# Performance work log

Hardware: AMD Instinct MI355X
Metric: run time of the kernel (lower is better)

Reference implementation:

```python
import jax, jax.numpy as jnp
import numpy as np

B, N, L, D = 16, 8192, 512, 384  # batch, points, latents, model dim
FF = 4 * D  # feedforward inner dim (after GEGLU split)


def _ln(x, g, b, eps=1e-5):
    m = jnp.mean(x, axis=-1, keepdims=True)
    v = jnp.mean((x - m) ** 2, axis=-1, keepdims=True)
    return (x - m) * jax.lax.rsqrt(v + eps) * g + b


def setup_inputs() -> dict:
    key = jax.random.key(0)
    ks = jax.random.split(key, 16)
    s = 0.02
    def w(k, shape):
        return jax.random.normal(k, shape, jnp.float32) * s
    return {
        "x": jax.random.normal(ks[0], (B, N, 3), jnp.float32),
        # MLP: in(3)->D, D->D, D->D, D->D with ReLU between (eqx-style depth=3)
        "mlp_w0": w(ks[1], (3, D)), "mlp_b0": jnp.zeros((D,), jnp.float32),
        "mlp_w1": w(ks[2], (D, D)), "mlp_b1": jnp.zeros((D,), jnp.float32),
        "mlp_w2": w(ks[3], (D, D)), "mlp_b2": jnp.zeros((D,), jnp.float32),
        "mlp_w3": w(ks[4], (D, D)), "mlp_b3": jnp.zeros((D,), jnp.float32),
        "query": jax.random.normal(ks[5], (1, L, D), jnp.float32),
        "ln_q_g": jnp.ones((D,), jnp.float32), "ln_q_b": jnp.zeros((D,), jnp.float32),
        "ln_ctx_g": jnp.ones((D,), jnp.float32), "ln_ctx_b": jnp.zeros((D,), jnp.float32),
        "wq": w(ks[6], (D, D)),
        "wkv": w(ks[7], (D, 2 * D)),
        "wo": w(ks[8], (D, D)), "bo": jnp.zeros((D,), jnp.float32),
        "ln_ff_g": jnp.ones((D,), jnp.float32), "ln_ff_b": jnp.zeros((D,), jnp.float32),
        "ff_w1": w(ks[9], (D, 2 * FF)), "ff_b1": jnp.zeros((2 * FF,), jnp.float32),
        "ff_w2": w(ks[10], (FF, D)), "ff_b2": jnp.zeros((D,), jnp.float32),
    }


def reference(x, mlp_w0, mlp_b0, mlp_w1, mlp_b1, mlp_w2, mlp_b2, mlp_w3, mlp_b3,
              query, ln_q_g, ln_q_b, ln_ctx_g, ln_ctx_b, wq, wkv, wo, bo,
              ln_ff_g, ln_ff_b, ff_w1, ff_b1, ff_w2, ff_b2):
    # point MLP: 3 -> D
    h = jax.nn.relu(x @ mlp_w0 + mlp_b0)
    h = jax.nn.relu(h @ mlp_w1 + mlp_b1)
    h = jax.nn.relu(h @ mlp_w2 + mlp_b2)
    ctx = h @ mlp_w3 + mlp_b3                      # [B, N, D]

    lq = jnp.broadcast_to(query, (x.shape[0], L, D))  # learnable latents

    # PreNorm cross-attention (heads=1, dim_head=D)
    qn = _ln(lq, ln_q_g, ln_q_b)
    cn = _ln(ctx, ln_ctx_g, ln_ctx_b)
    q = qn @ wq                                    # [B, L, D]
    kv = cn @ wkv
    k, v = jnp.split(kv, 2, axis=-1)               # [B, N, D] each
    scale = D ** -0.5
    sim = jnp.einsum('bid,bjd->bij', q, k) * scale # [B, L, N]
    attn = jax.nn.softmax(sim, axis=-1)
    out = jnp.einsum('bij,bjd->bid', attn, v)      # [B, L, D]
    x1 = (out @ wo + bo) + lq                      # residual

    # PreNorm GEGLU feedforward
    f = _ln(x1, ln_ff_g, ln_ff_b)
    f = f @ ff_w1 + ff_b1                          # [B, L, 2*FF]
    a, g = jnp.split(f, 2, axis=-1)
    f = a * jax.nn.gelu(g, approximate=False)      # GEGLU (exact gelu, torch default)
    return (f @ ff_w2 + ff_b2) + x1                # [B, L, D]
```

## Files before the change

### kernel.cpp

```cpp
#include <hip/hip_runtime.h>
#include <math.h>


typedef unsigned short u16;
typedef unsigned int   u32;
typedef __bf16 bf16_t;
typedef bf16_t bf16x8 __attribute__((ext_vector_type(8)));
typedef float  floatx4 __attribute__((ext_vector_type(4)));

__device__ __forceinline__ float b2f(u16 v) {
    return __uint_as_float(((u32)v) << 16);
}
__device__ __forceinline__ u16 f2b(float f) {
    bf16_t h = (bf16_t)f;
    return __builtin_bit_cast(u16, h);
}
__device__ __forceinline__ void stb4(u16* p, float4 f) {
    uint2 v;
    v.x = (u32)f2b(f.x) | ((u32)f2b(f.y) << 16);
    v.y = (u32)f2b(f.z) | ((u32)f2b(f.w) << 16);
    *(uint2*)p = v;
}

__device__ __forceinline__ void gl2lds16(u16* lds, const u16* g) {
    __builtin_amdgcn_global_load_lds(
        (const __attribute__((address_space(1))) void*)g,
        (__attribute__((address_space(3))) void*)lds, 16, 0, 0);
}

__device__ __forceinline__ void xcd_remap(int& bx, int& by, int& bz) {
    int gx = gridDim.x, gy = gridDim.y, gz = gridDim.z;
    int nb = gx * gy * gz;
    int p = bx + gx * (by + gy * bz);
    if ((nb & 7) == 0) {
        int chunk = nb >> 3;
        p = (p & 7) * chunk + (p >> 3);
    }
    bx = p % gx;
    int t = p / gx;
    by = t % gy;
    bz = t / gy;
}

__device__ __forceinline__ void xcd_remap_yf(int& bx, int& by, int& bz) {
    int gx = gridDim.x, gy = gridDim.y, gz = gridDim.z;
    int nb = gx * gy * gz;
    int p = by + gy * (bx + gx * bz);
    if ((nb & 7) == 0) {
        int chunk = nb >> 3;
        p = (p & 7) * chunk + (p >> 3);
    }
    by = p % gy;
    int t = p / gy;
    bx = t % gx;
    bz = t / gx;
}

__global__ __launch_bounds__(256) void wconv_all(
    const float* __restrict__ w1, const float* __restrict__ w2,
    const float* __restrict__ w3, const float* __restrict__ wq,
    const float* __restrict__ wkv, const float* __restrict__ wo,
    const float* __restrict__ ffw1, const float* __restrict__ ffw2,
    u16* __restrict__ d1, u16* __restrict__ d2, u16* __restrict__ d3,
    u16* __restrict__ dq, u16* __restrict__ dkv, u16* __restrict__ dо,
    u16* __restrict__ dffw1, u16* __restrict__ dffw2,
    u16* __restrict__ dwkd)
{
    int idx = blockIdx.x * 256 + threadIdx.x;
    if (idx >= 2949120) return;
    if (idx >= 2801664) {
        int local = idx - 2801664;
        int e = local / 384, d = local - e * 384;
        dwkd[local] = f2b(wkv[(long long)e * 768 + d]);
        return;
    }
    const float* W; u16* WT; int Kd, Nd, local;
    if      (idx <  147456) { W=w1;   WT=d1;    Kd=384;  Nd=384;  local=idx; }
    else if (idx <  294912) { W=w2;   WT=d2;    Kd=384;  Nd=384;  local=idx-147456; }
    else if (idx <  442368) { W=w3;   WT=d3;    Kd=384;  Nd=384;  local=idx-294912; }
    else if (idx <  589824) { W=wq;   WT=dq;    Kd=384;  Nd=384;  local=idx-442368; }
    else if (idx <  884736) { W=wkv;  WT=dkv;   Kd=384;  Nd=768;  local=idx-589824; }
    else if (idx < 1032192) { W=wo;   WT=dо;    Kd=384;  Nd=384;  local=idx-884736; }
    else if (idx < 2211840) { W=ffw1; WT=dffw1; Kd=384;  Nd=3072; local=idx-1032192; }
    else                    { W=ffw2; WT=dffw2; Kd=1536; Nd=384;  local=idx-2211840; }
    int n = local / Kd, k = local - n * Kd;
    WT[local] = f2b(W[(long long)k * Nd + n]);
}

__global__ __launch_bounds__(256) void layer0_kernel(
    const float* __restrict__ X, const float* __restrict__ W0,
    const float* __restrict__ B0, u16* __restrict__ H, int total4)
{
    int idx = blockIdx.x * 256 + threadIdx.x;
    if (idx >= total4) return;
    int e = idx * 4;
    int m = e / 384;
    int j = e - m * 384;
    float x0 = X[m * 3 + 0], x1 = X[m * 3 + 1], x2 = X[m * 3 + 2];
    float4 w0 = *(const float4*)(W0 + j);
    float4 w1 = *(const float4*)(W0 + 384 + j);
    float4 w2 = *(const float4*)(W0 + 768 + j);
    float4 bb = *(const float4*)(B0 + j);
    float4 v;
    v.x = fmaxf(bb.x + x0 * w0.x + x1 * w1.x + x2 * w2.x, 0.f);
    v.y = fmaxf(bb.y + x0 * w0.y + x1 * w1.y + x2 * w2.y, 0.f);
    v.z = fmaxf(bb.z + x0 * w0.z + x1 * w1.z + x2 * w2.z, 0.f);
    v.w = fmaxf(bb.w + x0 * w0.w + x1 * w1.w + x2 * w2.w, 0.f);
    stb4(H + e, v);
}

template<int IN_F32>
__global__ __launch_bounds__(256) void ln_kernel(
    const void* __restrict__ Xv, const float* __restrict__ g,
    const float* __restrict__ b, u16* __restrict__ Y, int rows)
{
    int w = threadIdx.x >> 6, lane = threadIdx.x & 63;
    int row = blockIdx.x * 4 + w;
    if (row >= rows) return;
    float v[6];
    float s = 0.f, ss = 0.f;
#pragma unroll
    for (int i = 0; i < 6; ++i) {
        int c = i * 64 + lane;
        v[i] = IN_F32 ? ((const float*)Xv)[(long long)row * 384 + c]
                      : b2f(((const u16*)Xv)[(long long)row * 384 + c]);
        s += v[i]; ss += v[i] * v[i];
    }
#pragma unroll
    for (int m = 32; m; m >>= 1) {
        s  += __shfl_xor(s, m, 64);
        ss += __shfl_xor(ss, m, 64);
    }
    float mean = s * (1.0f / 384.0f);
    float var  = ss * (1.0f / 384.0f) - mean * mean;
    float rs = rsqrtf(fmaxf(var, 0.f) + 1e-5f);
    u16* yr = Y + (long long)row * 384;
#pragma unroll
    for (int i = 0; i < 6; ++i) {
        int c = i * 64 + lane;
        yr[c] = f2b((v[i] - mean) * rs * g[c] + b[c]);
    }
}

#define STAGE_AB3(bufi, kk)                                                    \
    { u16* asd_ = shmem + (bufi) * 4096;                                       \
      u16* bsd_ = shmem + 12288 + (bufi) * 4096;                               \
      gl2lds16(asd_ + (wv * 32) * 32,                                          \
          aptr_ + (long long)(m0 + wv * 32 + rlo_) * lda_ + (kk) + c8_);       \
      gl2lds16(asd_ + (wv * 32 + 16) * 32,                                     \
          aptr_ + (long long)(m0 + wv * 32 + 16 + rlo_) * lda_ + (kk) + c8_);  \
      gl2lds16(bsd_ + (wv * 32) * 32,                                          \
          bptr_ + (long long)(n0 + wv * 32 + rlo_) * ldb_ + (kk) + c8_);       \
      gl2lds16(bsd_ + (wv * 32 + 16) * 32,                                     \
          bptr_ + (long long)(n0 + wv * 32 + 16 + rlo_) * ldb_ + (kk) + c8_); }

#define MFMA_TILE_PIPE(Aptr, Bptr, LDA, LDB, K0, K1)                           \
    {                                                                          \
        const u16* aptr_ = (Aptr); const u16* bptr_ = (Bptr);                  \
        const long long lda_ = (LDA), ldb_ = (LDB);                            \
        const int rlo_ = lane >> 2, c8_ = (lane & 3) * 8;                      \
        const int T_ = ((K1) - (K0)) >> 5;                                     \
        STAGE_AB3(0, (K0))                                                     \
        STAGE_AB3(1, (K0) + 32)                                                \
        int cur = 0;                                                           \
        for (int t = 0; t < T_; ++t) {                                         \
            if (t + 1 < T_) { asm volatile("s_waitcnt vmcnt(4)" ::: "memory"); } \
            else            { asm volatile("s_waitcnt vmcnt(0)" ::: "memory"); } \
            __builtin_amdgcn_s_barrier();                                      \
            if (t + 2 < T_) {                                                  \
                int stg = (cur == 0) ? 2 : cur - 1;                            \
                STAGE_AB3(stg, (K0) + (t + 2) * 32)                            \
            }                                                                  \
            const u16* As_ = shmem + cur * 4096;                               \
            const u16* Bs_ = shmem + 12288 + cur * 4096;                       \
            bf16x8 a0 = *(const bf16x8*)&As_[(wv * 32 + lr) * 32 + lq * 8];    \
            bf16x8 a1 = *(const bf16x8*)&As_[(wv * 32 + 16 + lr) * 32 + lq * 8]; \
            _Pragma("unroll")                                                  \
            for (int ns = 0; ns < 8; ++ns) {                                   \
                bf16x8 b = *(const bf16x8*)&Bs_[(ns * 16 + lr) * 32 + lq * 8]; \
                acc[0][ns] = __builtin_amdgcn_mfma_f32_16x16x32_bf16(a0, b, acc[0][ns], 0, 0, 0); \
                acc[1][ns] = __builtin_amdgcn_mfma_f32_16x16x32_bf16(a1, b, acc[1][ns], 0, 0, 0); \
            }                                                                  \
            cur = (cur == 2) ? 0 : cur + 1;                                    \
        }                                                                      \
    }

#define STAGE_AB2(bufi, kk)                                                    \
    { u16* asd_ = shmem + (bufi) * 4096;                                       \
      u16* bsd_ = shmem + 8192 + (bufi) * 4096;                                \
      gl2lds16(asd_ + (wv * 32) * 32,                                          \
          aptr_ + (long long)(m0 + wv * 32 + rlo_) * lda_ + (kk) + c8_);       \
      gl2lds16(asd_ + (wv * 32 + 16) * 32,                                     \
          aptr_ + (long long)(m0 + wv * 32 + 16 + rlo_) * lda_ + (kk) + c8_);  \
      gl2lds16(bsd_ + (wv * 32) * 32,                                          \
          bptr_ + (long long)(n0 + wv * 32 + rlo_) * ldb_ + (kk) + c8_);       \
      gl2lds16(bsd_ + (wv * 32 + 16) * 32,                                     \
          bptr_ + (long long)(n0 + wv * 32 + 16 + rlo_) * ldb_ + (kk) + c8_); }

#define MFMA_TILE_DBUF(Aptr, Bptr, LDA, LDB, K0, K1)                           \
    {                                                                          \
        const u16* aptr_ = (Aptr); const u16* bptr_ = (Bptr);                  \
        const long long lda_ = (LDA), ldb_ = (LDB);                            \
        const int rlo_ = lane >> 2, c8_ = (lane & 3) * 8;                      \
        int cur = 0;                                                           \
        STAGE_AB2(0, (K0))                                                     \
        for (int k0 = (K0); k0 < (K1); k0 += 32) {                             \
            __syncthreads();                                                   \
            if (k0 + 32 < (K1)) STAGE_AB2(cur ^ 1, k0 + 32)                    \
            const u16* As_ = shmem + cur * 4096;                               \
            const u16* Bs_ = shmem + 8192 + cur * 4096;                        \
            bf16x8 a0 = *(const bf16x8*)&As_[(wv * 32 + lr) * 32 + lq * 8];    \
            bf16x8 a1 = *(const bf16x8*)&As_[(wv * 32 + 16 + lr) * 32 + lq * 8]; \
            _Pragma("unroll")                                                  \
            for (int ns = 0; ns < 8; ++ns) {                                   \
                bf16x8 b = *(const bf16x8*)&Bs_[(ns * 16 + lr) * 32 + lq * 8]; \
                acc[0][ns] = __builtin_amdgcn_mfma_f32_16x16x32_bf16(a0, b, acc[0][ns], 0, 0, 0); \
                acc[1][ns] = __builtin_amdgcn_mfma_f32_16x16x32_bf16(a1, b, acc[1][ns], 0, 0, 0); \
            }                                                                  \
            cur ^= 1;                                                          \
        }                                                                      \
    }

template<int RES_F32, int OUT_F32>
__global__ __launch_bounds__(256) void gemm_mfma(
    const u16* __restrict__ A, const u16* __restrict__ WT,
    const float* __restrict__ bias, const void* __restrict__ res,
    void* __restrict__ C,
    int M, int N, int K, int lda, int ldb, int ldc, int ldres,
    float scale, int relu, int resmask,
    long long zsA, long long zsB, long long zsC)
{
    __shared__ u16 shmem[24576];
    const int tid = threadIdx.x;
    const int wv = tid >> 6, lane = tid & 63;
    const int lr = lane & 15, lq = lane >> 4;
    int bx = blockIdx.x, by = blockIdx.y, bz = blockIdx.z;
    xcd_remap_yf(bx, by, bz);
    const int m0 = bx * 128;
    const int n0 = by * 128;
    const u16* Az = A + bz * zsA;
    const u16* Bz = WT + bz * zsB;
    const long long czoff = bz * zsC;

    floatx4 acc[2][8];
#pragma unroll
    for (int i = 0; i < 2; ++i)
#pragma unroll
        for (int j = 0; j < 8; ++j)
            acc[i][j] = (floatx4){0.f, 0.f, 0.f, 0.f};

    MFMA_TILE_PIPE(Az, Bz, lda, ldb, 0, K)

    float bi[8];
#pragma unroll
    for (int ns = 0; ns < 8; ++ns)
        bi[ns] = bias ? bias[n0 + ns * 16 + lr] : 0.f;

#pragma unroll
    for (int ms = 0; ms < 2; ++ms) {
#pragma unroll
        for (int r = 0; r < 4; ++r) {
            int m = m0 + wv * 32 + ms * 16 + lq * 4 + r;
#pragma unroll
            for (int ns = 0; ns < 8; ++ns) {
                int col = n0 + ns * 16 + lr;
                float v = acc[ms][ns][r] * scale + bi[ns];
                if (relu) v = fmaxf(v, 0.f);
                if (res) {
                    long long ro = (long long)(m & resmask) * ldres + col;
                    v += RES_F32 ? ((const float*)res)[ro]
                                 : b2f(((const u16*)res)[ro]);
                }
                long long co = czoff + (long long)m * ldc + col;
                if (OUT_F32) ((float*)C)[co] = v;
                else         ((u16*)C)[co] = f2b(v);
            }
        }
    }
}

__global__ __launch_bounds__(256) void gemm_exp(
    const u16* __restrict__ A, const u16* __restrict__ WT,
    u16* __restrict__ P, float* __restrict__ den,
    int K, int lda, int ldb, int ldc,
    long long zsB, long long zsP)
{
    __shared__ u16 shmem[16384];
    const int tid = threadIdx.x;
    const int wv = tid >> 6, lane = tid & 63;
    const int lr = lane & 15, lq = lane >> 4;
    int bx = blockIdx.x, by = blockIdx.y, bz = blockIdx.z;
    xcd_remap(bx, by, bz);
    const int m0 = bx * 128;
    const int n0 = by * 128;
    const u16* Bz = WT + bz * zsB;
    u16* Pz = P + bz * zsP;
    float* dz = den + bz * 512;

    floatx4 acc[2][8];
#pragma unroll
    for (int i = 0; i < 2; ++i)
#pragma unroll
        for (int j = 0; j < 8; ++j)
            acc[i][j] = (floatx4){0.f, 0.f, 0.f, 0.f};

    MFMA_TILE_DBUF(A, Bz, lda, ldb, 0, K)

    u16* sh = shmem;
    float srow[2][4] = {};
#pragma unroll
    for (int ms = 0; ms < 2; ++ms) {
        __syncthreads();
#pragma unroll
        for (int ns = 0; ns < 8; ++ns)
#pragma unroll
            for (int r = 0; r < 4; ++r) {
                float l = acc[ms][ns][r];
                l = fminf(fmaxf(l, -60.f), 60.f);
                float p = __expf(l);
                srow[ms][r] += p;
                int row = wv * 16 + lq * 4 + r;
                int col = (ns * 16 + lr) ^ (((row >> 3) & 1) << 3);
                sh[row * 136 + col] = f2b(p);
            }
        __syncthreads();
#pragma unroll
        for (int j = 0; j < 4; ++j) {
            int idx = j * 256 + tid;
            int rl = idx >> 4, ch = idx & 15;
            int m = m0 + ((rl >> 4) << 5) + ms * 16 + (rl & 15);
            int src = rl * 136 + ((ch * 8) ^ ((((rl >> 3) & 1)) << 3));
            *(uint4*)&Pz[(long long)m * ldc + n0 + ch * 8] =
                *(const uint4*)&sh[src];
        }
    }
#pragma unroll
    for (int ms = 0; ms < 2; ++ms)
#pragma unroll
        for (int r = 0; r < 4; ++r) {
            float s = srow[ms][r];
            s += __shfl_xor(s, 1, 64);
            s += __shfl_xor(s, 2, 64);
            s += __shfl_xor(s, 4, 64);
            s += __shfl_xor(s, 8, 64);
            if (lr == 0)
                atomicAdd(&dz[m0 + wv * 32 + ms * 16 + lq * 4 + r], s);
        }
}

__global__ __launch_bounds__(256) void gemm_pv(
    const u16* __restrict__ P, const u16* __restrict__ VT,
    const float* __restrict__ den, u16* __restrict__ part, int SPLIT)
{
    __shared__ u16 shmem[24576];
    const int tid = threadIdx.x;
    const int wv = tid >> 6, lane = tid & 63;
    const int lr = lane & 15, lq = lane >> 4;
    int bx = blockIdx.x, by = blockIdx.y, bz = blockIdx.z;
    xcd_remap(bx, by, bz);
    const int m0 = bx * 128;
    const int n0 = by * 128;
    const int g = bz / SPLIT, sp = bz - g * SPLIT;
    const int chunk = 8192 / SPLIT;
    const u16* Az = P + (long long)g * 512 * 8192;
    const u16* Bz = VT + (long long)g * 384 * 8192;
    const float* dg = den + g * 512;

    floatx4 acc[2][8];
#pragma unroll
    for (int i = 0; i < 2; ++i)
#pragma unroll
        for (int j = 0; j < 8; ++j)
            acc[i][j] = (floatx4){0.f, 0.f, 0.f, 0.f};

    MFMA_TILE_PIPE(Az, Bz, 8192, 8192, sp * chunk, sp * chunk + chunk)

    u16* pz = part + (long long)bz * 512 * 384;
#pragma unroll
    for (int ms = 0; ms < 2; ++ms)
#pragma unroll
        for (int r = 0; r < 4; ++r) {
            int m = m0 + wv * 32 + ms * 16 + lq * 4 + r;
            float inv = 1.0f / dg[m];
#pragma unroll
            for (int ns = 0; ns < 8; ++ns) {
                int col = n0 + ns * 16 + lr;
                pz[(long long)m * 384 + col] = f2b(acc[ms][ns][r] * inv);
            }
        }
}

__global__ __launch_bounds__(256) void pv_reduce_kernel(
    const u16* __restrict__ part, u16* __restrict__ AO, int SPLIT)
{
    int idx = blockIdx.x * 256 + threadIdx.x;
    int q = idx / 96, j = (idx - q * 96) * 4;
    int g = q >> 9, ql = q & 511;
    const u16* base = part + ((long long)g * SPLIT * 512 + ql) * 384 + j;
    float4 s = make_float4(0.f, 0.f, 0.f, 0.f);
    for (int sp = 0; sp < SPLIT; ++sp) {
        uint2 v = *(const uint2*)(base + (long long)sp * 512 * 384);
        s.x += b2f((u16)(v.x & 0xffff));
        s.y += b2f((u16)(v.x >> 16));
        s.z += b2f((u16)(v.y & 0xffff));
        s.w += b2f((u16)(v.y >> 16));
    }
    stb4(AO + (long long)q * 384 + j, s);
}

__global__ __launch_bounds__(256) void gemm_ff1_geglu(
    const u16* __restrict__ A, const u16* __restrict__ WT,
    const float* __restrict__ bias, u16* __restrict__ C,
    int K, int lda, int ldb, int ldc)
{
    __shared__ u16 shmem[24576];
    const int tid = threadIdx.x;
    const int wv = tid >> 6, lane = tid & 63;
    const int lr = lane & 15, lq = lane >> 4;
    int bx = blockIdx.x, by = blockIdx.y, bz = blockIdx.z;
    xcd_remap_yf(bx, by, bz);
    const int m0 = bx * 128;
    const int n0 = by * 64;
    const int rlo = lane >> 2, c8 = (lane & 3) * 8;

    floatx4 accA[2][4], accG[2][4];
#pragma unroll
    for (int i = 0; i < 2; ++i)
#pragma unroll
        for (int j = 0; j < 4; ++j) {
            accA[i][j] = (floatx4){0.f, 0.f, 0.f, 0.f};
            accG[i][j] = (floatx4){0.f, 0.f, 0.f, 0.f};
        }

#define STAGE_FF(bufi, kk)                                                     \
    { u16* asd = shmem + (bufi) * 4096;                                        \
      u16* bsd = shmem + 12288 + (bufi) * 4096;                                \
      gl2lds16(asd + (wv * 32) * 32,                                           \
          A + (long long)(m0 + wv * 32 + rlo) * lda + (kk) + c8);              \
      gl2lds16(asd + (wv * 32 + 16) * 32,                                      \
          A + (long long)(m0 + wv * 32 + 16 + rlo) * lda + (kk) + c8);         \
      int r0 = wv * 32 + rlo, r1 = r0 + 16;                                    \
      int wrow0 = (r0 < 64) ? (n0 + r0) : (1536 + n0 + r0 - 64);               \
      int wrow1 = (r1 < 64) ? (n0 + r1) : (1536 + n0 + r1 - 64);               \
      gl2lds16(bsd + (wv * 32) * 32, WT + (long long)wrow0 * ldb + (kk) + c8); \
      gl2lds16(bsd + (wv * 32 + 16) * 32, WT + (long long)wrow1 * ldb + (kk) + c8); }

    const int T = K >> 5;
    STAGE_FF(0, 0)
    STAGE_FF(1, 32)
    int cur = 0;
    for (int t = 0; t < T; ++t) {
        if (t + 1 < T) { asm volatile("s_waitcnt vmcnt(4)" ::: "memory"); }
        else           { asm volatile("s_waitcnt vmcnt(0)" ::: "memory"); }
        __builtin_amdgcn_s_barrier();
        if (t + 2 < T) {
            int stg = (cur == 0) ? 2 : cur - 1;
            STAGE_FF(stg, (t + 2) * 32)
        }
        const u16* As_ = shmem + cur * 4096;
        const u16* Bs_ = shmem + 12288 + cur * 4096;
        bf16x8 a0 = *(const bf16x8*)&As_[(wv * 32 + lr) * 32 + lq * 8];
        bf16x8 a1 = *(const bf16x8*)&As_[(wv * 32 + 16 + lr) * 32 + lq * 8];
#pragma unroll
        for (int ns = 0; ns < 4; ++ns) {
            bf16x8 bA = *(const bf16x8*)&Bs_[(ns * 16 + lr) * 32 + lq * 8];
            bf16x8 bG = *(const bf16x8*)&Bs_[((64 + ns * 16) + lr) * 32 + lq * 8];
            accA[0][ns] = __builtin_amdgcn_mfma_f32_16x16x32_bf16(a0, bA, accA[0][ns], 0, 0, 0);
            accA[1][ns] = __builtin_amdgcn_mfma_f32_16x16x32_bf16(a1, bA, accA[1][ns], 0, 0, 0);
            accG[0][ns] = __builtin_amdgcn_mfma_f32_16x16x32_bf16(a0, bG, accG[0][ns], 0, 0, 0);
            accG[1][ns] = __builtin_amdgcn_mfma_f32_16x16x32_bf16(a1, bG, accG[1][ns], 0, 0, 0);
        }
        cur = (cur == 2) ? 0 : cur + 1;
    }
#undef STAGE_FF

    float ba[4], bg[4];
#pragma unroll
    for (int ns = 0; ns < 4; ++ns) {
        ba[ns] = bias[n0 + ns * 16 + lr];
        bg[ns] = bias[1536 + n0 + ns * 16 + lr];
    }
#pragma unroll
    for (int ms = 0; ms < 2; ++ms)
#pragma unroll
        for (int r = 0; r < 4; ++r) {
            int m = m0 + wv * 32 + ms * 16 + lq * 4 + r;
#pragma unroll
            for (int ns = 0; ns < 4; ++ns) {
                int col = n0 + ns * 16 + lr;
                float a = accA[ms][ns][r] + ba[ns];
                float g = accG[ms][ns][r] + bg[ns];
                float v = a * 0.5f * g * (1.0f + erff(g * 0.70710678118654752f));
                C[(long long)m * ldc + col] = f2b(v);
            }
        }
}

extern "C" void kernel_launch(void* const* d_in, const int* in_sizes, int n_in,
                              void* d_out, int out_size, void* d_ws, size_t ws_size,
                              hipStream_t stream) {
    const float* x     = (const float*)d_in[0];
    const float* w0    = (const float*)d_in[1];
    const float* b0    = (const float*)d_in[2];
    const float* w1    = (const float*)d_in[3];
    const float* b1    = (const float*)d_in[4];
    const float* w2    = (const float*)d_in[5];
    const float* b2    = (const float*)d_in[6];
    const float* w3    = (const float*)d_in[7];
    const float* b3    = (const float*)d_in[8];
    const float* query = (const float*)d_in[9];
    const float* lnqg  = (const float*)d_in[10];
    const float* lnqb  = (const float*)d_in[11];
    const float* lncg  = (const float*)d_in[12];
    const float* lncb  = (const float*)d_in[13];
    const float* wq    = (const float*)d_in[14];
    const float* wkv   = (const float*)d_in[15];
    const float* wo    = (const float*)d_in[16];
    const float* bo    = (const float*)d_in[17];
    const float* lnfg  = (const float*)d_in[18];
    const float* lnfb  = (const float*)d_in[19];
    const float* ffw1  = (const float*)d_in[20];
    const float* ffb1  = (const float*)d_in[21];
    const float* ffw2  = (const float*)d_in[22];
    const float* ffb2  = (const float*)d_in[23];
    float* out = (float*)d_out;
    char* wsb = (char*)d_ws;

    auto need = [](int G) -> size_t {
        return (size_t)G * (3LL * 6291456 + 8388608)
             + 25165824
             + 6291456
             + 3 * 393216 + 32768
             + 5898240;
    };
    int G = 2;
    if      (ws_size >= need(16)) G = 16;
    else if (ws_size >= need(8))  G = 8;
    else if (ws_size >= need(4))  G = 4;
    const int SPLIT = 64 / G;

    long long off = 0;
    u16*   bufA   = (u16*)(wsb + off); off += (long long)G * 6291456;
    u16*   bufB   = (u16*)(wsb + off); off += (long long)G * 6291456;
    u16*   VTb    = (u16*)(wsb + off); off += (long long)G * 6291456;
    u16*   Pb     = (u16*)(wsb + off); off += (long long)G * 8388608;
    u16*   part   = (u16*)(wsb + off); off += 25165824;
    u16*   ao_all = (u16*)(wsb + off); off += 6291456;
    u16*   qn     = (u16*)(wsb + off); off += 393216;
    u16*   qb     = (u16*)(wsb + off); off += 393216;
    u16*   q2     = (u16*)(wsb + off); off += 393216;
    float* den    = (float*)(wsb + off); off += 32768;
    u16*   w1T    = (u16*)(wsb + off); off += 294912;
    u16*   w2T    = (u16*)(wsb + off); off += 294912;
    u16*   w3T    = (u16*)(wsb + off); off += 294912;
    u16*   wqT    = (u16*)(wsb + off); off += 294912;
    u16*   wkvT   = (u16*)(wsb + off); off += 589824;
    u16*   woT    = (u16*)(wsb + off); off += 294912;
    u16*   ffw1T  = (u16*)(wsb + off); off += 2359296;
    u16*   ffw2T  = (u16*)(wsb + off); off += 1179648;
    u16*   wkdir  = (u16*)(wsb + off); off += 294912;
    u16*   x1_all = (u16*)(wsb + 0);
    u16*   f0_all = (u16*)(wsb + 6291456);
    u16*   gl_all = (u16*)(wsb + 12582912);

    const int FULLMASK = 0x3FFFFFFF;

    wconv_all<<<11520, 256, 0, stream>>>(w1, w2, w3, wq, wkv, wo, ffw1, ffw2,
        w1T, w2T, w3T, wqT, wkvT, woT, ffw1T, ffw2T, wkdir);
    hipMemsetAsync(den, 0, 16 * 512 * sizeof(float), stream);
    ln_kernel<1><<<128, 256, 0, stream>>>(query, lnqg, lnqb, qn, 512);
    gemm_mfma<0, 0><<<dim3(4, 3), 256, 0, stream>>>(qn, wqT, nullptr, nullptr, qb,
        512, 384, 384, 384, 384, 384, 0, 1.f, 0, FULLMASK, 0, 0, 0);
    gemm_mfma<0, 0><<<dim3(4, 3), 256, 0, stream>>>(qb, wkdir, nullptr, nullptr, q2,
        512, 384, 384, 384, 384, 384, 0, 0.05103103630798288f, 0, FULLMASK, 0, 0, 0);

    const int MG = G * 8192;
    for (int base = 0; base < 16; base += G) {
        const float* xg = x + (long long)base * 24576;

        layer0_kernel<<<G * 3072, 256, 0, stream>>>(xg, w0, b0, bufA, G * 786432);
        gemm_mfma<0, 0><<<dim3(MG / 128, 3), 256, 0, stream>>>(bufA, w1T, b1, nullptr, bufB,
            MG, 384, 384, 384, 384, 384, 0, 1.f, 1, FULLMASK, 0, 0, 0);
        gemm_mfma<0, 0><<<dim3(MG / 128, 3), 256, 0, stream>>>(bufB, w2T, b2, nullptr, bufA,
            MG, 384, 384, 384, 384, 384, 0, 1.f, 1, FULLMASK, 0, 0, 0);
        gemm_mfma<0, 0><<<dim3(MG / 128, 3), 256, 0, stream>>>(bufA, w3T, b3, nullptr, bufB,
            MG, 384, 384, 384, 384, 384, 0, 1.f, 0, FULLMASK, 0, 0, 0);
        ln_kernel<0><<<MG / 4, 256, 0, stream>>>(bufB, lncg, lncb, bufA, MG);
        gemm_mfma<0, 0><<<dim3(3, 64, G), 256, 0, stream>>>(wkvT + 147456, bufA,
            nullptr, nullptr, VTb, 384, 8192, 384, 384, 384, 8192, 0, 1.f, 0, FULLMASK,
            0, 8192LL * 384, 384LL * 8192);
        gemm_exp<<<dim3(4, 64, G), 256, 0, stream>>>(q2, bufA, Pb, den + base * 512,
            384, 384, 384, 8192, 8192LL * 384, 512LL * 8192);
        gemm_pv<<<dim3(4, 3, G * SPLIT), 256, 0, stream>>>(Pb, VTb, den + base * 512,
            part, SPLIT);
        pv_reduce_kernel<<<G * 192, 256, 0, stream>>>(part,
            ao_all + (long long)base * 196608, SPLIT);
    }

    gemm_mfma<1, 0><<<dim3(64, 3), 256, 0, stream>>>(ao_all, woT, bo, query, x1_all,
        8192, 384, 384, 384, 384, 384, 384, 1.f, 0, 511, 0, 0, 0);
    ln_kernel<0><<<2048, 256, 0, stream>>>(x1_all, lnfg, lnfb, f0_all, 8192);
    gemm_ff1_geglu<<<dim3(64, 24), 256, 0, stream>>>(f0_all, ffw1T, ffb1, gl_all,
        384, 384, 384, 1536);
    gemm_mfma<0, 1><<<dim3(64, 3), 256, 0, stream>>>(gl_all, ffw2T, ffb2, x1_all, out,
        8192, 384, 1536, 1536, 1536, 384, 384, 1.f, 0, FULLMASK, 0, 0, 0);
}
```

Measured before the change: 786.6 us.

## Fold value projection into output projection and fuse LN with transpose

Applies associativity: attention output times Wv times Wo is computed as attention output times a precomputed (Wv·Wo) matrix, so the per-batch V projection GEMM over all 8192 points is removed. The PV GEMM now consumes the transposed normalized context directly, and a new layernorm kernel writes both the normalized rows and their transpose through shared memory. This adds one small 384x384 weight GEMM and a strided transposed store, and changes bf16 rounding order slightly.

```diff
diff --git a/kernel.cpp b/kernel.cpp
--- a/kernel.cpp
+++ b/kernel.cpp
@@ -62,14 +62,20 @@
     const float* __restrict__ wkv, const float* __restrict__ wo,
     const float* __restrict__ ffw1, const float* __restrict__ ffw2,
     u16* __restrict__ d1, u16* __restrict__ d2, u16* __restrict__ d3,
-    u16* __restrict__ dq, u16* __restrict__ dkv, u16* __restrict__ dо,
+    u16* __restrict__ dq, u16* __restrict__ dо,
     u16* __restrict__ dffw1, u16* __restrict__ dffw2,
-    u16* __restrict__ dwkd)
+    u16* __restrict__ dwkd, u16* __restrict__ dwvd)
 {
     int idx = blockIdx.x * 256 + threadIdx.x;
-    if (idx >= 2949120) return;
-    if (idx >= 2801664) {
-        int local = idx - 2801664;
+    if (idx >= 2801664) return;
+    if (idx >= 2654208) {
+        int local = idx - 2654208;
+        int dd = local / 384, c = local - dd * 384;
+        dwvd[local] = f2b(wkv[(long long)dd * 768 + 384 + c]);
+        return;
+    }
+    if (idx >= 2506752) {
+        int local = idx - 2506752;
         int e = local / 384, d = local - e * 384;
         dwkd[local] = f2b(wkv[(long long)e * 768 + d]);
         return;
@@ -79,10 +85,9 @@
     else if (idx <  294912) { W=w2;   WT=d2;    Kd=384;  Nd=384;  local=idx-147456; }
     else if (idx <  442368) { W=w3;   WT=d3;    Kd=384;  Nd=384;  local=idx-294912; }
     else if (idx <  589824) { W=wq;   WT=dq;    Kd=384;  Nd=384;  local=idx-442368; }
-    else if (idx <  884736) { W=wkv;  WT=dkv;   Kd=384;  Nd=768;  local=idx-589824; }
-    else if (idx < 1032192) { W=wo;   WT=dо;    Kd=384;  Nd=384;  local=idx-884736; }
-    else if (idx < 2211840) { W=ffw1; WT=dffw1; Kd=384;  Nd=3072; local=idx-1032192; }
-    else                    { W=ffw2; WT=dffw2; Kd=1536; Nd=384;  local=idx-2211840; }
+    else if (idx <  737280) { W=wo;   WT=dо;    Kd=384;  Nd=384;  local=idx-589824; }
+    else if (idx < 1916928) { W=ffw1; WT=dffw1; Kd=384;  Nd=3072; local=idx-737280; }
+    else                    { W=ffw2; WT=dffw2; Kd=1536; Nd=384;  local=idx-1916928; }
     int n = local / Kd, k = local - n * Kd;
     WT[local] = f2b(W[(long long)k * Nd + n]);
 }
@@ -139,6 +144,54 @@
     for (int i = 0; i < 6; ++i) {
         int c = i * 64 + lane;
         yr[c] = f2b((v[i] - mean) * rs * g[c] + b[c]);
+    }
+}
+
+__global__ __launch_bounds__(256) void ln_tr_kernel(
+    const u16* __restrict__ Xv, const float* __restrict__ g,
+    const float* __restrict__ b, u16* __restrict__ Y, u16* __restrict__ YT)
+{
+    __shared__ u16 tr[384 * 72];
+    int w = threadIdx.x >> 6, lane = threadIdx.x & 63;
+    int row0 = blockIdx.x * 64;
+    for (int rr = 0; rr < 16; ++rr) {
+        int jl = w * 16 + rr;
+        long long row = row0 + jl;
+        float v[6];
+        float s = 0.f, ss = 0.f;
+#pragma unroll
+        for (int i = 0; i < 6; ++i) {
+            int c = i * 64 + lane;
+            v[i] = b2f(Xv[row * 384 + c]);
+            s += v[i]; ss += v[i] * v[i];
+        }
+#pragma unroll
+        for (int m = 32; m; m >>= 1) {
+            s  += __shfl_xor(s, m, 64);
+            ss += __shfl_xor(ss, m, 64);
+        }
+        float mean = s * (1.0f / 384.0f);
+        float var  = ss * (1.0f / 384.0f) - mean * mean;
+        float rs = rsqrtf(fmaxf(var, 0.f) + 1e-5f);
+        u16* yr = Y + row * 384;
+#pragma unroll
+        for (int i = 0; i < 6; ++i) {
+            int c = i * 64 + lane;
+            u16 val = f2b((v[i] - mean) * rs * g[c] + b[c]);
+            yr[c] = val;
+            tr[c * 72 + jl] = val;
+        }
+    }
+    __syncthreads();
+    int gb = row0 >> 13;
+    int jloc = row0 & 8191;
+    u16* yt = YT + (long long)gb * 384 * 8192 + jloc;
+    for (int e = threadIdx.x; e < 384; e += 256) {
+        const u16* src = &tr[e * 72];
+        u16* dst = yt + (long long)e * 8192;
+#pragma unroll
+        for (int q = 0; q < 8; ++q)
+            *(uint4*)(dst + q * 8) = *(const uint4*)(src + q * 8);
     }
 }
 
@@ -349,7 +402,7 @@
 }
 
 __global__ __launch_bounds__(256) void gemm_pv(
-    const u16* __restrict__ P, const u16* __restrict__ VT,
+    const u16* __restrict__ P, const u16* __restrict__ KT,
     const float* __restrict__ den, u16* __restrict__ part, int SPLIT)
 {
     __shared__ u16 shmem[24576];
@@ -363,7 +416,7 @@
     const int g = bz / SPLIT, sp = bz - g * SPLIT;
     const int chunk = 8192 / SPLIT;
     const u16* Az = P + (long long)g * 512 * 8192;
-    const u16* Bz = VT + (long long)g * 384 * 8192;
+    const u16* Bz = KT + (long long)g * 384 * 8192;
     const float* dg = den + g * 512;
 
     floatx4 acc[2][8];
@@ -542,7 +595,7 @@
     long long off = 0;
     u16*   bufA   = (u16*)(wsb + off); off += (long long)G * 6291456;
     u16*   bufB   = (u16*)(wsb + off); off += (long long)G * 6291456;
-    u16*   VTb    = (u16*)(wsb + off); off += (long long)G * 6291456;
+    u16*   knT    = (u16*)(wsb + off); off += (long long)G * 6291456;
     u16*   Pb     = (u16*)(wsb + off); off += (long long)G * 8388608;
     u16*   part   = (u16*)(wsb + off); off += 25165824;
     u16*   ao_all = (u16*)(wsb + off); off += 6291456;
@@ -554,25 +607,28 @@
     u16*   w2T    = (u16*)(wsb + off); off += 294912;
     u16*   w3T    = (u16*)(wsb + off); off += 294912;
     u16*   wqT    = (u16*)(wsb + off); off += 294912;
-    u16*   wkvT   = (u16*)(wsb + off); off += 589824;
     u16*   woT    = (u16*)(wsb + off); off += 294912;
     u16*   ffw1T  = (u16*)(wsb + off); off += 2359296;
     u16*   ffw2T  = (u16*)(wsb + off); off += 1179648;
     u16*   wkdir  = (u16*)(wsb + off); off += 294912;
+    u16*   wvdir  = (u16*)(wsb + off); off += 294912;
+    u16*   wvoT   = (u16*)(wsb + off); off += 294912;
     u16*   x1_all = (u16*)(wsb + 0);
     u16*   f0_all = (u16*)(wsb + 6291456);
     u16*   gl_all = (u16*)(wsb + 12582912);
 
     const int FULLMASK = 0x3FFFFFFF;
 
-    wconv_all<<<11520, 256, 0, stream>>>(w1, w2, w3, wq, wkv, wo, ffw1, ffw2,
-        w1T, w2T, w3T, wqT, wkvT, woT, ffw1T, ffw2T, wkdir);
+    wconv_all<<<10944, 256, 0, stream>>>(w1, w2, w3, wq, wkv, wo, ffw1, ffw2,
+        w1T, w2T, w3T, wqT, woT, ffw1T, ffw2T, wkdir, wvdir);
     hipMemsetAsync(den, 0, 16 * 512 * sizeof(float), stream);
     ln_kernel<1><<<128, 256, 0, stream>>>(query, lnqg, lnqb, qn, 512);
     gemm_mfma<0, 0><<<dim3(4, 3), 256, 0, stream>>>(qn, wqT, nullptr, nullptr, qb,
         512, 384, 384, 384, 384, 384, 0, 1.f, 0, FULLMASK, 0, 0, 0);
     gemm_mfma<0, 0><<<dim3(4, 3), 256, 0, stream>>>(qb, wkdir, nullptr, nullptr, q2,
         512, 384, 384, 384, 384, 384, 0, 0.05103103630798288f, 0, FULLMASK, 0, 0, 0);
+    gemm_mfma<0, 0><<<dim3(3, 3), 256, 0, stream>>>(woT, wvdir, nullptr, nullptr, wvoT,
+        384, 384, 384, 384, 384, 384, 0, 1.f, 0, FULLMASK, 0, 0, 0);
 
     const int MG = G * 8192;
     for (int base = 0; base < 16; base += G) {
@@ -585,19 +641,16 @@
             MG, 384, 384, 384, 384, 384, 0, 1.f, 1, FULLMASK, 0, 0, 0);
         gemm_mfma<0, 0><<<dim3(MG / 128, 3), 256, 0, stream>>>(bufA, w3T, b3, nullptr, bufB,
             MG, 384, 384, 384, 384, 384, 0, 1.f, 0, FULLMASK, 0, 0, 0);
-        ln_kernel<0><<<MG / 4, 256, 0, stream>>>(bufB, lncg, lncb, bufA, MG);
-        gemm_mfma<0, 0><<<dim3(3, 64, G), 256, 0, stream>>>(wkvT + 147456, bufA,
-            nullptr, nullptr, VTb, 384, 8192, 384, 384, 384, 8192, 0, 1.f, 0, FULLMASK,
-            0, 8192LL * 384, 384LL * 8192);
+        ln_tr_kernel<<<MG / 64, 256, 0, stream>>>(bufB, lncg, lncb, bufA, knT);
         gemm_exp<<<dim3(4, 64, G), 256, 0, stream>>>(q2, bufA, Pb, den + base * 512,
             384, 384, 384, 8192, 8192LL * 384, 512LL * 8192);
-        gemm_pv<<<dim3(4, 3, G * SPLIT), 256, 0, stream>>>(Pb, VTb, den + base * 512,
+        gemm_pv<<<dim3(4, 3, G * SPLIT), 256, 0, stream>>>(Pb, knT, den + base * 512,
             part, SPLIT);
         pv_reduce_kernel<<<G * 192, 256, 0, stream>>>(part,
             ao_all + (long long)base * 196608, SPLIT);
     }
 
-    gemm_mfma<1, 0><<<dim3(64, 3), 256, 0, stream>>>(ao_all, woT, bo, query, x1_all,
+    gemm_mfma<1, 0><<<dim3(64, 3), 256, 0, stream>>>(ao_all, wvoT, bo, query, x1_all,
         8192, 384, 384, 384, 384, 384, 384, 1.f, 0, 511, 0, 0, 0);
     ln_kernel<0><<<2048, 256, 0, stream>>>(x1_all, lnfg, lnfb, f0_all, 8192);
     gemm_ff1_geglu<<<dim3(64, 24), 256, 0, stream>>>(f0_all, ffw1T, ffb1, gl_all,
```

After: 766.8 us, median of 2. -2.5%, faster.
